# Performance work log

Hardware: AMD Instinct MI355X
Metric: run time of the kernel (lower is better)

The kernel has to match this reference:

```python
import jax, jax.numpy as jnp
import numpy as np

N = 100000
E = 1600000
IN_C = 128
OUT_C = 64
NEG_SLOPE = 0.2


def setup_inputs() -> dict:
    key = jax.random.key(0)
    k1, k2, k3, k4 = jax.random.split(key, 4)
    x = jax.random.normal(k1, (N, IN_C), dtype=jnp.float32)
    edge_index = jax.random.randint(k2, (2, E), 0, N, dtype=jnp.int64)
    # Linear weight as in torch nn.Linear (bias=False): W @ x -> x @ W.T
    W = jax.random.normal(k3, (OUT_C, IN_C), dtype=jnp.float32) * (1.0 / np.sqrt(IN_C))
    # attention vector a over [Wx_i || Wx_j]
    a = jax.random.normal(k4, (2 * OUT_C,), dtype=jnp.float32) * (1.0 / np.sqrt(2 * OUT_C))
    return {"x": x, "edge_index": edge_index, "W": W, "a": a}


def reference(x, edge_index, W, a):
    src = edge_index[0]  # [E] source nodes j
    dst = edge_index[1]  # [E] target nodes i

    Wx = x @ W.T                                   # [N, OUT_C]
    # per-node attention scores, gathered per edge (same math as a . [Wx_i||Wx_j])
    s_i = Wx @ a[:OUT_C]                           # [N]
    s_j = Wx @ a[OUT_C:]                           # [N]
    e = jax.nn.leaky_relu(s_i[dst] + s_j[src], NEG_SLOPE)  # [E]

    # segment softmax over edges grouped by target node
    m = jax.ops.segment_max(e, dst, num_segments=N)        # [N]
    m = jnp.where(jnp.isneginf(m), 0.0, m)
    exp_e = jnp.exp(e - m[dst])                            # [E]
    denom = jax.ops.segment_sum(exp_e, dst, num_segments=N)  # [N]
    alpha = exp_e / denom[dst]                             # [E]

    msg = alpha[:, None] * Wx[src]                 # [E, OUT_C]
    h = jax.ops.segment_sum(msg, dst, num_segments=N)  # [N, OUT_C]
    return jax.nn.elu(h)
```

## Files before the change

### kernel.cpp

```cpp
#include <hip/hip_runtime.h>

#define NN 100000
#define EE 1600000
#define INC 128
#define OUTC 64
#define NEG_SLOPE 0.2f

#define BSH 7
#define BNODES 128
#define NB 782
#define BCAP 2560
#define SCAP2 4480
#define CHUNKA 4096
#define NBLKA 391
#define NSLOT 10

typedef __attribute__((ext_vector_type(8))) short bf16x8;
typedef __attribute__((ext_vector_type(4))) float f32x4;

__device__ __forceinline__ unsigned short f2bf(float f) {
  unsigned u = __float_as_uint(f);
  unsigned r = (u + 0x7fffu + ((u >> 16) & 1u)) >> 16;
  return (unsigned short)r;
}
__device__ __forceinline__ float bf2f(unsigned u16) {
  return __uint_as_float(u16 << 16);
}

__global__ __launch_bounds__(256) void k_gemm(
    const float* __restrict__ x, const float* __restrict__ W,
    const float* __restrict__ a, unsigned short* __restrict__ Wxh,
    float* __restrict__ s_i, float* __restrict__ s_j,
    int* __restrict__ gcursor)
{
  __shared__ __align__(16) unsigned short hs[4][32][72];
  const int t = threadIdx.x;
  const int w = t >> 6;
  const int l = t & 63;
  const int lr = l & 15;
  const int lk = l >> 4;
  const int row0 = blockIdx.x * 128 + w * 32;

  if (blockIdx.x == 0) {
    for (int i = t; i < NB; i += 256) gcursor[i] = 0;
  }

  f32x4 acc[2][4];
  #pragma unroll
  for (int m = 0; m < 2; ++m)
    #pragma unroll
    for (int n = 0; n < 4; ++n) acc[m][n] = (f32x4){0.f, 0.f, 0.f, 0.f};

  #pragma unroll
  for (int ks = 0; ks < 4; ++ks) {
    const int k0 = ks * 32 + lk * 8;
    bf16x8 af[2], bfr[4];
    #pragma unroll
    for (int m = 0; m < 2; ++m) {
      int r = row0 + m * 16 + lr;
      r = (r < NN) ? r : (NN - 1);
      const float* p = &x[(size_t)r * INC + k0];
      float4 u0 = *reinterpret_cast<const float4*>(p);
      float4 u1 = *reinterpret_cast<const float4*>(p + 4);
      af[m][0] = (short)f2bf(u0.x); af[m][1] = (short)f2bf(u0.y);
      af[m][2] = (short)f2bf(u0.z); af[m][3] = (short)f2bf(u0.w);
      af[m][4] = (short)f2bf(u1.x); af[m][5] = (short)f2bf(u1.y);
      af[m][6] = (short)f2bf(u1.z); af[m][7] = (short)f2bf(u1.w);
    }
    #pragma unroll
    for (int n = 0; n < 4; ++n) {
      int c = n * 16 + lr;
      const float* p = &W[(size_t)c * INC + k0];
      float4 u0 = *reinterpret_cast<const float4*>(p);
      float4 u1 = *reinterpret_cast<const float4*>(p + 4);
      bfr[n][0] = (short)f2bf(u0.x); bfr[n][1] = (short)f2bf(u0.y);
      bfr[n][2] = (short)f2bf(u0.z); bfr[n][3] = (short)f2bf(u0.w);
      bfr[n][4] = (short)f2bf(u1.x); bfr[n][5] = (short)f2bf(u1.y);
      bfr[n][6] = (short)f2bf(u1.z); bfr[n][7] = (short)f2bf(u1.w);
    }
    #pragma unroll
    for (int m = 0; m < 2; ++m)
      #pragma unroll
      for (int n = 0; n < 4; ++n)
        acc[m][n] = __builtin_amdgcn_mfma_f32_16x16x32_bf16(af[m], bfr[n], acc[m][n], 0, 0, 0);
  }

  float a1[4], a2[4];
  #pragma unroll
  for (int n = 0; n < 4; ++n) {
    a1[n] = a[n * 16 + lr];
    a2[n] = a[OUTC + n * 16 + lr];
  }
  #pragma unroll
  for (int m = 0; m < 2; ++m)
    #pragma unroll
    for (int r = 0; r < 4; ++r) {
      float p1 = 0.f, p2 = 0.f;
      #pragma unroll
      for (int n = 0; n < 4; ++n) {
        p1 = fmaf(acc[m][n][r], a1[n], p1);
        p2 = fmaf(acc[m][n][r], a2[n], p2);
      }
      #pragma unroll
      for (int mm = 1; mm < 16; mm <<= 1) {
        p1 += __shfl_xor(p1, mm);
        p2 += __shfl_xor(p2, mm);
      }
      int rr = row0 + m * 16 + lk * 4 + r;
      if (lr == 0 && rr < NN) { s_i[rr] = p1; s_j[rr] = p2; }
    }

  #pragma unroll
  for (int m = 0; m < 2; ++m)
    #pragma unroll
    for (int n = 0; n < 4; ++n)
      #pragma unroll
      for (int r = 0; r < 4; ++r)
        hs[w][m * 16 + lk * 4 + r][n * 16 + lr] = f2bf(acc[m][n][r]);
  __syncthreads();
  #pragma unroll
  for (int j = 0; j < 4; ++j) {
    int idx = j * 64 + l;
    int rr = idx >> 3;
    int c8 = idx & 7;
    int node = row0 + rr;
    if (node < NN) {
      uint4 v = *reinterpret_cast<const uint4*>(&hs[w][rr][c8 * 8]);
      *reinterpret_cast<uint4*>(&Wxh[(size_t)node * OUTC + c8 * 8]) = v;
    }
  }
}

__global__ __launch_bounds__(512) void k_bin(const int* __restrict__ src, const int* __restrict__ dst,
                                             int* __restrict__ gcursor, unsigned* __restrict__ binned) {
  __shared__ int lh[1024];
  __shared__ int ls[1024];
  __shared__ int gb[NB];
  __shared__ int wsum[8];
  __shared__ uint2 stage[CHUNKA];
  const int t = threadIdx.x;
  const int c0 = blockIdx.x * CHUNKA;
  const int cend = min(c0 + CHUNKA, EE);
  const int total = cend - c0;

  lh[t] = 0; lh[t + 512] = 0;
  __syncthreads();

  int esrc[8], edst[8], rnk[8];
  #pragma unroll
  for (int k = 0; k < 8; ++k) {
    int i = c0 + t + k * 512;
    bool v = i < cend;
    esrc[k] = v ? src[i] : -1;
    edst[k] = v ? dst[i] : -1;
    rnk[k] = v ? atomicAdd(&lh[edst[k] >> BSH], 1) : 0;
  }
  __syncthreads();

  {
    int a0 = lh[2 * t], a1 = lh[2 * t + 1];
    int s2 = a0 + a1;
    int incl = s2;
    #pragma unroll
    for (int d = 1; d < 64; d <<= 1) {
      int u = __shfl_up(incl, d);
      if ((t & 63) >= d) incl += u;
    }
    if ((t & 63) == 63) wsum[t >> 6] = incl;
    __syncthreads();
    int wv = t >> 6;
    int wbase = 0;
    #pragma unroll
    for (int k = 0; k < 8; ++k) wbase += (k < wv) ? wsum[k] : 0;
    int ex = wbase + incl - s2;
    ls[2 * t] = ex;
    ls[2 * t + 1] = ex + a0;
  }
  __syncthreads();

  #pragma unroll
  for (int k = 0; k < 8; ++k) {
    if (edst[k] >= 0) {
      int bb = edst[k] >> BSH;
      stage[ls[bb] + rnk[k]] =
          make_uint2((unsigned)esrc[k] | ((unsigned)(edst[k] & (BNODES - 1)) << 17),
                     (unsigned)bb);
    }
  }
  __syncthreads();

  for (int b = t; b < NB; b += 512) {
    int cnt = lh[b];
    if (cnt) gb[b] = atomicAdd(&gcursor[b], cnt);
  }
  __syncthreads();

  for (int i = t; i < total; i += 512) {
    uint2 pr = stage[i];
    int b = (int)pr.y;
    int idx = gb[b] + (i - ls[b]);
    if (idx < BCAP) binned[b * BCAP + idx] = pr.x;
  }
}

__global__ __launch_bounds__(256) void k_sort(const int* __restrict__ gcursor,
                                              const unsigned* __restrict__ binned,
                                              const float* __restrict__ s_i,
                                              const float* __restrict__ s_j,
                                              uint2* __restrict__ offs2,
                                              unsigned* __restrict__ sorted4) {
  __shared__ int cnt128[BNODES];
  __shared__ int ex128[BNODES];
  __shared__ float sil[BNODES];
  __shared__ float den[BNODES];
  __shared__ float invd[BNODES];
  __shared__ unsigned stage[SCAP2];
  __shared__ int sW0, sTot;
  const int t = threadIdx.x;
  const int b = blockIdx.x;
  const int n0 = b << BSH;
  const int base = b * BCAP;
  const int obase = b * SCAP2;
  const int cnt = min(gcursor[b], BCAP);

  for (int i = t; i < SCAP2; i += 256) stage[i] = 0u;
  if (t < BNODES) {
    cnt128[t] = 0;
    den[t] = 0.f;
    int n = n0 + t;
    sil[t] = (n < NN) ? s_i[n] : 0.f;
  }
  __syncthreads();

  unsigned es[NSLOT];
  int ed[NSLOT], rk[NSLOT];
  float ws[NSLOT];
  #pragma unroll
  for (int k = 0; k < NSLOT; ++k) {
    int i = t + k * 256;
    bool v = i < cnt;
    unsigned pw = v ? binned[base + i] : 0u;
    es[k] = pw & 0x1ffffu;
    ed[k] = v ? (int)(pw >> 17) : -1;
    ws[k] = 0.f;
    rk[k] = 0;
    if (v) {
      rk[k] = atomicAdd(&cnt128[ed[k]], 1);
      float sc = sil[ed[k]] + s_j[es[k]];
      sc = (sc > 0.f) ? sc : NEG_SLOPE * sc;
      ws[k] = __expf(sc);
      atomicAdd(&den[ed[k]], ws[k]);
    }
  }
  __syncthreads();

  int cpad = 0;
  if (t < BNODES) {
    float dv = den[t];
    invd[t] = (dv > 0.f) ? 1.f / dv : 0.f;
    cpad = (cnt128[t] + 15) & ~15;
  }
  int incl = cpad;
  #pragma unroll
  for (int d = 1; d < 64; d <<= 1) {
    int u = __shfl_up(incl, d);
    if ((t & 63) >= d) incl += u;
  }
  if (t == 63) sW0 = incl;
  __syncthreads();
  if (t < BNODES) {
    int ex = incl - cpad + ((t >= 64) ? sW0 : 0);
    ex128[t] = ex;
    int n = n0 + t;
    if (n < NN) offs2[n] = make_uint2((unsigned)(obase + ex), (unsigned)(obase + ex + cnt128[t]));
    if (t == BNODES - 1) sTot = ex + cpad;
  }
  __syncthreads();

  #pragma unroll
  for (int k = 0; k < NSLOT; ++k) {
    if (ed[k] >= 0) {
      float alpha = ws[k] * invd[ed[k]];
      unsigned abits = (__float_as_uint(alpha) + 0x10000u) & 0xfffe0000u;
      stage[ex128[ed[k]] + rk[k]] = abits | es[k];
    }
  }
  __syncthreads();
  const int tot = sTot;
  for (int i = t; i < tot; i += 256) sorted4[obase + i] = stage[i];
}

__global__ __launch_bounds__(256) void k_aggregate(
    const uint2* __restrict__ offs2, const unsigned* __restrict__ sorted4,
    const unsigned short* __restrict__ Wxh, float* __restrict__ out)
{
  int n = blockIdx.x * 8 + (threadIdx.x >> 5);
  if (n >= NN) return;
  int l32 = threadIdx.x & 31;
  int g = l32 >> 3;
  unsigned cl8 = (l32 & 7) << 3;
  uint2 se = offs2[n];
  int start = (int)se.x, end = (int)se.y;
  float acc[8];
  #pragma unroll
  for (int j = 0; j < 8; ++j) acc[j] = 0.f;

  for (int base = start; base < end; base += 16) {
    int i = base + 4 * g;
    uint4 pw = *reinterpret_cast<const uint4*>(&sorted4[i]);
    unsigned s0 = pw.x & 0x1ffffu, s1 = pw.y & 0x1ffffu;
    unsigned s2 = pw.z & 0x1ffffu, s3 = pw.w & 0x1ffffu;
    float w0 = __uint_as_float(pw.x & 0xfffe0000u);
    float w1 = __uint_as_float(pw.y & 0xfffe0000u);
    float w2 = __uint_as_float(pw.z & 0xfffe0000u);
    float w3 = __uint_as_float(pw.w & 0xfffe0000u);
    uint4 h0 = *reinterpret_cast<const uint4*>(&Wxh[(s0 << 6) + cl8]);
    uint4 h1 = *reinterpret_cast<const uint4*>(&Wxh[(s1 << 6) + cl8]);
    uint4 h2 = *reinterpret_cast<const uint4*>(&Wxh[(s2 << 6) + cl8]);
    uint4 h3 = *reinterpret_cast<const uint4*>(&Wxh[(s3 << 6) + cl8]);
    acc[0] = fmaf(w0, bf2f(h0.x & 0xffffu), acc[0]);
    acc[1] = fmaf(w0, bf2f(h0.x >> 16), acc[1]);
    acc[2] = fmaf(w0, bf2f(h0.y & 0xffffu), acc[2]);
    acc[3] = fmaf(w0, bf2f(h0.y >> 16), acc[3]);
    acc[4] = fmaf(w0, bf2f(h0.z & 0xffffu), acc[4]);
    acc[5] = fmaf(w0, bf2f(h0.z >> 16), acc[5]);
    acc[6] = fmaf(w0, bf2f(h0.w & 0xffffu), acc[6]);
    acc[7] = fmaf(w0, bf2f(h0.w >> 16), acc[7]);
    acc[0] = fmaf(w1, bf2f(h1.x & 0xffffu), acc[0]);
    acc[1] = fmaf(w1, bf2f(h1.x >> 16), acc[1]);
    acc[2] = fmaf(w1, bf2f(h1.y & 0xffffu), acc[2]);
    acc[3] = fmaf(w1, bf2f(h1.y >> 16), acc[3]);
    acc[4] = fmaf(w1, bf2f(h1.z & 0xffffu), acc[4]);
    acc[5] = fmaf(w1, bf2f(h1.z >> 16), acc[5]);
    acc[6] = fmaf(w1, bf2f(h1.w & 0xffffu), acc[6]);
    acc[7] = fmaf(w1, bf2f(h1.w >> 16), acc[7]);
    acc[0] = fmaf(w2, bf2f(h2.x & 0xffffu), acc[0]);
    acc[1] = fmaf(w2, bf2f(h2.x >> 16), acc[1]);
    acc[2] = fmaf(w2, bf2f(h2.y & 0xffffu), acc[2]);
    acc[3] = fmaf(w2, bf2f(h2.y >> 16), acc[3]);
    acc[4] = fmaf(w2, bf2f(h2.z & 0xffffu), acc[4]);
    acc[5] = fmaf(w2, bf2f(h2.z >> 16), acc[5]);
    acc[6] = fmaf(w2, bf2f(h2.w & 0xffffu), acc[6]);
    acc[7] = fmaf(w2, bf2f(h2.w >> 16), acc[7]);
    acc[0] = fmaf(w3, bf2f(h3.x & 0xffffu), acc[0]);
    acc[1] = fmaf(w3, bf2f(h3.x >> 16), acc[1]);
    acc[2] = fmaf(w3, bf2f(h3.y & 0xffffu), acc[2]);
    acc[3] = fmaf(w3, bf2f(h3.y >> 16), acc[3]);
    acc[4] = fmaf(w3, bf2f(h3.z & 0xffffu), acc[4]);
    acc[5] = fmaf(w3, bf2f(h3.z >> 16), acc[5]);
    acc[6] = fmaf(w3, bf2f(h3.w & 0xffffu), acc[6]);
    acc[7] = fmaf(w3, bf2f(h3.w >> 16), acc[7]);
  }

  #pragma unroll
  for (int m = 8; m <= 16; m <<= 1) {
    #pragma unroll
    for (int j = 0; j < 8; ++j) acc[j] += __shfl_xor(acc[j], m);
  }

  if (g == 0) {
    float r[8];
    #pragma unroll
    for (int j = 0; j < 8; ++j)
      r[j] = (acc[j] > 0.f) ? acc[j] : __expf(acc[j]) - 1.f;
    float4 o0 = make_float4(r[0], r[1], r[2], r[3]);
    float4 o1 = make_float4(r[4], r[5], r[6], r[7]);
    unsigned ob = ((unsigned)n << 6) + cl8;
    *reinterpret_cast<float4*>(&out[ob]) = o0;
    *reinterpret_cast<float4*>(&out[ob + 4]) = o1;
  }
}

extern "C" void kernel_launch(void* const* d_in, const int* in_sizes, int n_in,
                              void* d_out, int out_size, void* d_ws, size_t ws_size,
                              hipStream_t stream) {
  const float* x = (const float*)d_in[0];
  const int* edge = (const int*)d_in[1];
  const float* W = (const float*)d_in[2];
  const float* a = (const float*)d_in[3];
  const int* srcIdx = edge;
  const int* dstIdx = edge + EE;
  float* out = (float*)d_out;

  unsigned short* Wxh = (unsigned short*)d_ws;
  unsigned* binned = (unsigned*)((char*)d_ws + (size_t)NN * OUTC * 2);
  unsigned* sorted4 = binned + (size_t)NB * BCAP;
  int* gcursor = (int*)(sorted4 + (size_t)NB * SCAP2);
  float* s_i = (float*)(gcursor + NB);
  float* s_j = s_i + NN;
  uint2* offs2 = (uint2*)(s_j + NN);

  k_gemm<<<NB, 256, 0, stream>>>(x, W, a, Wxh, s_i, s_j, gcursor);
  k_bin<<<NBLKA, 512, 0, stream>>>(srcIdx, dstIdx, gcursor, binned);
  k_sort<<<NB, 256, 0, stream>>>(gcursor, binned, s_i, s_j, offs2, sorted4);
  k_aggregate<<<(NN + 7) / 8, 256, 0, stream>>>(offs2, sorted4, Wxh, out);
}
```

Before: 96.81 us.

## Run GEMM and edge binning concurrently in one fused kernel launch

The GEMM and edge-binning kernels become one launch with a block-index split: the first NB blocks compute Wx and the attention scores, and the rest bin edges by destination bucket. The two phases are independent, so they can overlap on the GPU, removing a serialization point and a launch gap. The binning blocks now use 256 threads over 2048 edges each with a reworked scan, and shared memory is unioned into one buffer. A separate tiny kernel now zeros the global cursors, which adds a launch, and the union sizes shared memory to the larger of the two phases.

```diff
diff --git a/kernel.cpp b/kernel.cpp
--- a/kernel.cpp
+++ b/kernel.cpp
@@ -11,8 +11,8 @@
 #define NB 782
 #define BCAP 2560
 #define SCAP2 4480
-#define CHUNKA 4096
-#define NBLKA 391
+#define CHUNKB 2048
+#define NBLKB 782
 #define NSLOT 10
 
 typedef __attribute__((ext_vector_type(8))) short bf16x8;
@@ -27,179 +27,183 @@
   return __uint_as_float(u16 << 16);
 }
 
-__global__ __launch_bounds__(256) void k_gemm(
+__global__ __launch_bounds__(256) void k_zero(int* __restrict__ gcursor) {
+  for (int i = threadIdx.x; i < NB; i += 256) gcursor[i] = 0;
+}
+
+__global__ __launch_bounds__(256) void k_fused(
     const float* __restrict__ x, const float* __restrict__ W,
     const float* __restrict__ a, unsigned short* __restrict__ Wxh,
     float* __restrict__ s_i, float* __restrict__ s_j,
-    int* __restrict__ gcursor)
+    const int* __restrict__ src, const int* __restrict__ dst,
+    int* __restrict__ gcursor, unsigned* __restrict__ binned)
 {
-  __shared__ __align__(16) unsigned short hs[4][32][72];
+  __shared__ __align__(16) char smem[27728];
   const int t = threadIdx.x;
-  const int w = t >> 6;
-  const int l = t & 63;
-  const int lr = l & 15;
-  const int lk = l >> 4;
-  const int row0 = blockIdx.x * 128 + w * 32;
-
-  if (blockIdx.x == 0) {
-    for (int i = t; i < NB; i += 256) gcursor[i] = 0;
-  }
-
-  f32x4 acc[2][4];
-  #pragma unroll
-  for (int m = 0; m < 2; ++m)
-    #pragma unroll
-    for (int n = 0; n < 4; ++n) acc[m][n] = (f32x4){0.f, 0.f, 0.f, 0.f};
-
-  #pragma unroll
-  for (int ks = 0; ks < 4; ++ks) {
-    const int k0 = ks * 32 + lk * 8;
-    bf16x8 af[2], bfr[4];
-    #pragma unroll
-    for (int m = 0; m < 2; ++m) {
-      int r = row0 + m * 16 + lr;
-      r = (r < NN) ? r : (NN - 1);
-      const float* p = &x[(size_t)r * INC + k0];
-      float4 u0 = *reinterpret_cast<const float4*>(p);
-      float4 u1 = *reinterpret_cast<const float4*>(p + 4);
-      af[m][0] = (short)f2bf(u0.x); af[m][1] = (short)f2bf(u0.y);
-      af[m][2] = (short)f2bf(u0.z); af[m][3] = (short)f2bf(u0.w);
-      af[m][4] = (short)f2bf(u1.x); af[m][5] = (short)f2bf(u1.y);
-      af[m][6] = (short)f2bf(u1.z); af[m][7] = (short)f2bf(u1.w);
-    }
+
+  if (blockIdx.x < NB) {
+    unsigned short (*hs)[32][72] = reinterpret_cast<unsigned short(*)[32][72]>(smem);
+    const int w = t >> 6;
+    const int l = t & 63;
+    const int lr = l & 15;
+    const int lk = l >> 4;
+    const int row0 = blockIdx.x * 128 + w * 32;
+
+    f32x4 acc[2][4];
+    #pragma unroll
+    for (int m = 0; m < 2; ++m)
+      #pragma unroll
+      for (int n = 0; n < 4; ++n) acc[m][n] = (f32x4){0.f, 0.f, 0.f, 0.f};
+
+    #pragma unroll
+    for (int ks = 0; ks < 4; ++ks) {
+      const int k0 = ks * 32 + lk * 8;
+      bf16x8 af[2], bfr[4];
+      #pragma unroll
+      for (int m = 0; m < 2; ++m) {
+        int r = row0 + m * 16 + lr;
+        r = (r < NN) ? r : (NN - 1);
+        const float* p = &x[(size_t)r * INC + k0];
+        float4 u0 = *reinterpret_cast<const float4*>(p);
+        float4 u1 = *reinterpret_cast<const float4*>(p + 4);
+        af[m][0] = (short)f2bf(u0.x); af[m][1] = (short)f2bf(u0.y);
+        af[m][2] = (short)f2bf(u0.z); af[m][3] = (short)f2bf(u0.w);
+        af[m][4] = (short)f2bf(u1.x); af[m][5] = (short)f2bf(u1.y);
+        af[m][6] = (short)f2bf(u1.z); af[m][7] = (short)f2bf(u1.w);
+      }
+      #pragma unroll
+      for (int n = 0; n < 4; ++n) {
+        int c = n * 16 + lr;
+        const float* p = &W[(size_t)c * INC + k0];
+        float4 u0 = *reinterpret_cast<const float4*>(p);
+        float4 u1 = *reinterpret_cast<const float4*>(p + 4);
+        bfr[n][0] = (short)f2bf(u0.x); bfr[n][1] = (short)f2bf(u0.y);
+        bfr[n][2] = (short)f2bf(u0.z); bfr[n][3] = (short)f2bf(u0.w);
+        bfr[n][4] = (short)f2bf(u1.x); bfr[n][5] = (short)f2bf(u1.y);
+        bfr[n][6] = (short)f2bf(u1.z); bfr[n][7] = (short)f2bf(u1.w);
+      }
+      #pragma unroll
+      for (int m = 0; m < 2; ++m)
+        #pragma unroll
+        for (int n = 0; n < 4; ++n)
+          acc[m][n] = __builtin_amdgcn_mfma_f32_16x16x32_bf16(af[m], bfr[n], acc[m][n], 0, 0, 0);
+    }
+
+    float a1[4], a2[4];
     #pragma unroll
     for (int n = 0; n < 4; ++n) {
-      int c = n * 16 + lr;
-      const float* p = &W[(size_t)c * INC + k0];
-      float4 u0 = *reinterpret_cast<const float4*>(p);
-      float4 u1 = *reinterpret_cast<const float4*>(p + 4);
-      bfr[n][0] = (short)f2bf(u0.x); bfr[n][1] = (short)f2bf(u0.y);
-      bfr[n][2] = (short)f2bf(u0.z); bfr[n][3] = (short)f2bf(u0.w);
-      bfr[n][4] = (short)f2bf(u1.x); bfr[n][5] = (short)f2bf(u1.y);
-      bfr[n][6] = (short)f2bf(u1.z); bfr[n][7] = (short)f2bf(u1.w);
+      a1[n] = a[n * 16 + lr];
+      a2[n] = a[OUTC + n * 16 + lr];
     }
     #pragma unroll
     for (int m = 0; m < 2; ++m)
       #pragma unroll
+      for (int r = 0; r < 4; ++r) {
+        float p1 = 0.f, p2 = 0.f;
+        #pragma unroll
+        for (int n = 0; n < 4; ++n) {
+          p1 = fmaf(acc[m][n][r], a1[n], p1);
+          p2 = fmaf(acc[m][n][r], a2[n], p2);
+        }
+        #pragma unroll
+        for (int mm = 1; mm < 16; mm <<= 1) {
+          p1 += __shfl_xor(p1, mm);
+          p2 += __shfl_xor(p2, mm);
+        }
+        int rr = row0 + m * 16 + lk * 4 + r;
+        if (lr == 0 && rr < NN) { s_i[rr] = p1; s_j[rr] = p2; }
+      }
+
+    #pragma unroll
+    for (int m = 0; m < 2; ++m)
+      #pragma unroll
       for (int n = 0; n < 4; ++n)
-        acc[m][n] = __builtin_amdgcn_mfma_f32_16x16x32_bf16(af[m], bfr[n], acc[m][n], 0, 0, 0);
-  }
-
-  float a1[4], a2[4];
-  #pragma unroll
-  for (int n = 0; n < 4; ++n) {
-    a1[n] = a[n * 16 + lr];
-    a2[n] = a[OUTC + n * 16 + lr];
-  }
-  #pragma unroll
-  for (int m = 0; m < 2; ++m)
-    #pragma unroll
-    for (int r = 0; r < 4; ++r) {
-      float p1 = 0.f, p2 = 0.f;
-      #pragma unroll
-      for (int n = 0; n < 4; ++n) {
-        p1 = fmaf(acc[m][n][r], a1[n], p1);
-        p2 = fmaf(acc[m][n][r], a2[n], p2);
-      }
-      #pragma unroll
-      for (int mm = 1; mm < 16; mm <<= 1) {
-        p1 += __shfl_xor(p1, mm);
-        p2 += __shfl_xor(p2, mm);
-      }
-      int rr = row0 + m * 16 + lk * 4 + r;
-      if (lr == 0 && rr < NN) { s_i[rr] = p1; s_j[rr] = p2; }
-    }
-
-  #pragma unroll
-  for (int m = 0; m < 2; ++m)
-    #pragma unroll
-    for (int n = 0; n < 4; ++n)
-      #pragma unroll
-      for (int r = 0; r < 4; ++r)
-        hs[w][m * 16 + lk * 4 + r][n * 16 + lr] = f2bf(acc[m][n][r]);
-  __syncthreads();
-  #pragma unroll
-  for (int j = 0; j < 4; ++j) {
-    int idx = j * 64 + l;
-    int rr = idx >> 3;
-    int c8 = idx & 7;
-    int node = row0 + rr;
-    if (node < NN) {
-      uint4 v = *reinterpret_cast<const uint4*>(&hs[w][rr][c8 * 8]);
-      *reinterpret_cast<uint4*>(&Wxh[(size_t)node * OUTC + c8 * 8]) = v;
-    }
-  }
-}
-
-__global__ __launch_bounds__(512) void k_bin(const int* __restrict__ src, const int* __restrict__ dst,
-                                             int* __restrict__ gcursor, unsigned* __restrict__ binned) {
-  __shared__ int lh[1024];
-  __shared__ int ls[1024];
-  __shared__ int gb[NB];
-  __shared__ int wsum[8];
-  __shared__ uint2 stage[CHUNKA];
-  const int t = threadIdx.x;
-  const int c0 = blockIdx.x * CHUNKA;
-  const int cend = min(c0 + CHUNKA, EE);
-  const int total = cend - c0;
-
-  lh[t] = 0; lh[t + 512] = 0;
-  __syncthreads();
-
-  int esrc[8], edst[8], rnk[8];
-  #pragma unroll
-  for (int k = 0; k < 8; ++k) {
-    int i = c0 + t + k * 512;
-    bool v = i < cend;
-    esrc[k] = v ? src[i] : -1;
-    edst[k] = v ? dst[i] : -1;
-    rnk[k] = v ? atomicAdd(&lh[edst[k] >> BSH], 1) : 0;
-  }
-  __syncthreads();
-
-  {
-    int a0 = lh[2 * t], a1 = lh[2 * t + 1];
-    int s2 = a0 + a1;
-    int incl = s2;
-    #pragma unroll
-    for (int d = 1; d < 64; d <<= 1) {
-      int u = __shfl_up(incl, d);
-      if ((t & 63) >= d) incl += u;
-    }
-    if ((t & 63) == 63) wsum[t >> 6] = incl;
-    __syncthreads();
-    int wv = t >> 6;
-    int wbase = 0;
-    #pragma unroll
-    for (int k = 0; k < 8; ++k) wbase += (k < wv) ? wsum[k] : 0;
-    int ex = wbase + incl - s2;
-    ls[2 * t] = ex;
-    ls[2 * t + 1] = ex + a0;
-  }
-  __syncthreads();
-
-  #pragma unroll
-  for (int k = 0; k < 8; ++k) {
-    if (edst[k] >= 0) {
-      int bb = edst[k] >> BSH;
-      stage[ls[bb] + rnk[k]] =
-          make_uint2((unsigned)esrc[k] | ((unsigned)(edst[k] & (BNODES - 1)) << 17),
-                     (unsigned)bb);
-    }
-  }
-  __syncthreads();
-
-  for (int b = t; b < NB; b += 512) {
-    int cnt = lh[b];
-    if (cnt) gb[b] = atomicAdd(&gcursor[b], cnt);
-  }
-  __syncthreads();
-
-  for (int i = t; i < total; i += 512) {
-    uint2 pr = stage[i];
-    int b = (int)pr.y;
-    int idx = gb[b] + (i - ls[b]);
-    if (idx < BCAP) binned[b * BCAP + idx] = pr.x;
+        #pragma unroll
+        for (int r = 0; r < 4; ++r)
+          hs[w][m * 16 + lk * 4 + r][n * 16 + lr] = f2bf(acc[m][n][r]);
+    __syncthreads();
+    #pragma unroll
+    for (int j = 0; j < 4; ++j) {
+      int idx = j * 64 + l;
+      int rr = idx >> 3;
+      int c8 = idx & 7;
+      int node = row0 + rr;
+      if (node < NN) {
+        uint4 v = *reinterpret_cast<const uint4*>(&hs[w][rr][c8 * 8]);
+        *reinterpret_cast<uint4*>(&Wxh[(size_t)node * OUTC + c8 * 8]) = v;
+      }
+    }
+  } else {
+    int* lh = reinterpret_cast<int*>(smem);
+    int* ls = lh + 1024;
+    int* gb = ls + 1024;
+    uint2* stage = reinterpret_cast<uint2*>(smem + 11344);
+    __shared__ int wsum[4];
+    const int c0 = (blockIdx.x - NB) * CHUNKB;
+    const int cend = min(c0 + CHUNKB, EE);
+    const int total = cend - c0;
+
+    #pragma unroll
+    for (int k = 0; k < 4; ++k) lh[t + k * 256] = 0;
+    __syncthreads();
+
+    int esrc[8], edst[8], rnk[8];
+    #pragma unroll
+    for (int k = 0; k < 8; ++k) {
+      int i = c0 + t + k * 256;
+      bool v = i < cend;
+      esrc[k] = v ? src[i] : -1;
+      edst[k] = v ? dst[i] : -1;
+      rnk[k] = v ? atomicAdd(&lh[edst[k] >> BSH], 1) : 0;
+    }
+    __syncthreads();
+
+    {
+      int a0 = lh[4 * t], a1 = lh[4 * t + 1], a2 = lh[4 * t + 2], a3 = lh[4 * t + 3];
+      int s4 = a0 + a1 + a2 + a3;
+      int incl = s4;
+      #pragma unroll
+      for (int d = 1; d < 64; d <<= 1) {
+        int u = __shfl_up(incl, d);
+        if ((t & 63) >= d) incl += u;
+      }
+      if ((t & 63) == 63) wsum[t >> 6] = incl;
+      __syncthreads();
+      int wv = t >> 6;
+      int wbase = 0;
+      #pragma unroll
+      for (int k = 0; k < 4; ++k) wbase += (k < wv) ? wsum[k] : 0;
+      int ex = wbase + incl - s4;
+      ls[4 * t] = ex;
+      ls[4 * t + 1] = ex + a0;
+      ls[4 * t + 2] = ex + a0 + a1;
+      ls[4 * t + 3] = ex + a0 + a1 + a2;
+    }
+    __syncthreads();
+
+    #pragma unroll
+    for (int k = 0; k < 8; ++k) {
+      if (edst[k] >= 0) {
+        int bb = edst[k] >> BSH;
+        stage[ls[bb] + rnk[k]] =
+            make_uint2((unsigned)esrc[k] | ((unsigned)(edst[k] & (BNODES - 1)) << 17),
+                       (unsigned)bb);
+      }
+    }
+    __syncthreads();
+
+    for (int b = t; b < NB; b += 256) {
+      int cnt = lh[b];
+      if (cnt) gb[b] = atomicAdd(&gcursor[b], cnt);
+    }
+    __syncthreads();
+
+    for (int i = t; i < total; i += 256) {
+      uint2 pr = stage[i];
+      int b = (int)pr.y;
+      int idx = gb[b] + (i - ls[b]);
+      if (idx < BCAP) binned[b * BCAP + idx] = pr.x;
+    }
   }
 }
 
@@ -390,8 +394,9 @@
   float* s_j = s_i + NN;
   uint2* offs2 = (uint2*)(s_j + NN);
 
-  k_gemm<<<NB, 256, 0, stream>>>(x, W, a, Wxh, s_i, s_j, gcursor);
-  k_bin<<<NBLKA, 512, 0, stream>>>(srcIdx, dstIdx, gcursor, binned);
+  k_zero<<<1, 256, 0, stream>>>(gcursor);
+  k_fused<<<NB + NBLKB, 256, 0, stream>>>(x, W, a, Wxh, s_i, s_j,
+                                          srcIdx, dstIdx, gcursor, binned);
   k_sort<<<NB, 256, 0, stream>>>(gcursor, binned, s_i, s_j, offs2, sorted4);
   k_aggregate<<<(NN + 7) / 8, 256, 0, stream>>>(offs2, sorted4, Wxh, out);
 }
```

Result: slower. 98.95 us (+2.2%).
